# Kernel optimization log

Measured on AMD Instinct MI355X. Metric: run time of the kernel, lower is better.

## Reference

```python
import jax, jax.numpy as jnp
import numpy as np

E = 30      # embedding_dim
H = 3       # num_heads
D = E // H  # head_dim = 10
EPS = 1e-5


def setup_inputs() -> dict:
    key = jax.random.key(0)
    ks = jax.random.split(key, 16)
    B = 1_000_000
    s = 0.1
    return {
        "input": jax.random.normal(ks[0], (B, 2, 5), dtype=jnp.float32),
        "w_emb": jax.random.normal(ks[1], (E, 5), dtype=jnp.float32) * s,
        "b_emb": jax.random.normal(ks[2], (E,), dtype=jnp.float32) * s,
        "w_in": jax.random.normal(ks[3], (3 * E, E), dtype=jnp.float32) * s,
        "b_in": jax.random.normal(ks[4], (3 * E,), dtype=jnp.float32) * s,
        "w_out": jax.random.normal(ks[5], (E, E), dtype=jnp.float32) * s,
        "b_out": jax.random.normal(ks[6], (E,), dtype=jnp.float32) * s,
        "w1": jax.random.normal(ks[7], (E, E), dtype=jnp.float32) * s,
        "b1": jax.random.normal(ks[8], (E,), dtype=jnp.float32) * s,
        "w2": jax.random.normal(ks[9], (E, E), dtype=jnp.float32) * s,
        "b2": jax.random.normal(ks[10], (E,), dtype=jnp.float32) * s,
        "gamma": jnp.ones((E,), dtype=jnp.float32),
        "beta": jnp.zeros((E,), dtype=jnp.float32),
        "w_o": jax.random.normal(ks[11], (3, E), dtype=jnp.float32) * s,
        "b_o": jax.random.normal(ks[12], (3,), dtype=jnp.float32) * s,
    }


def _layernorm(x, gamma, beta):
    mu = jnp.mean(x, axis=-1, keepdims=True)
    var = jnp.var(x, axis=-1, keepdims=True)
    return (x - mu) * jax.lax.rsqrt(var + EPS) * gamma + beta


def reference(input, w_emb, b_emb, w_in, b_in, w_out, b_out,
              w1, b1, w2, b2, gamma, beta, w_o, b_o):
    B = input.shape[0]
    # embed both tokens: [B,2,5] -> [B,2,E], exact (erf) GELU as in torch default
    x = jax.nn.gelu(jnp.einsum('bse,de->bsd', input, w_emb) + b_emb,
                    approximate=False)
    # MHA (torch nn.MultiheadAttention, batch_first)
    qkv = jnp.einsum('bsd,fd->bsf', x, w_in) + b_in  # [B,2,3E]
    q, k, v = jnp.split(qkv, 3, axis=-1)
    # [B,2,E] -> [B,H,2,D]
    q = q.reshape(B, 2, H, D).transpose(0, 2, 1, 3)
    k = k.reshape(B, 2, H, D).transpose(0, 2, 1, 3)
    v = v.reshape(B, 2, H, D).transpose(0, 2, 1, 3)
    scores = jnp.einsum('bhqd,bhkd->bhqk', q, k) / jnp.sqrt(jnp.float32(D))
    attn = jax.nn.softmax(scores, axis=-1)
    ctx = jnp.einsum('bhqk,bhkd->bhqd', attn, v)  # [B,H,2,D]
    ctx = ctx.transpose(0, 2, 1, 3).reshape(B, 2, E)
    attn_out = jnp.einsum('bsd,fd->bsf', ctx, w_out) + b_out
    out = _layernorm(attn_out + x, gamma, beta)
    # FFN (applied per token, same weights)
    h = jax.nn.gelu(jnp.einsum('bsd,fd->bsf', out, w1) + b1, approximate=False)
    fc_out = jnp.einsum('bsd,fd->bsf', h, w2) + b2
    out = _layernorm(out + fc_out, gamma, beta)  # same norm1 params reused
    logits = jnp.einsum('bsd,od->bso', out, w_o) + b_o
    return logits[:, 1, :]
```

## Files before the change

kernel.cpp:

```cpp
#include <hip/hip_runtime.h>
#include <math.h>


typedef _Float16 h8 __attribute__((ext_vector_type(8)));
typedef _Float16 h2v __attribute__((ext_vector_type(2)));
typedef float f4 __attribute__((ext_vector_type(4)));
typedef f4 f4u __attribute__((aligned(4)));

#define EPS 1e-5f
#define GDEG 9

struct GeluCU { unsigned c[GDEG + 2]; };

__device__ __forceinline__ f4 MF(h8 a, h8 b, f4 c) {
    return __builtin_amdgcn_mfma_f32_16x16x32_f16(a, b, c, 0, 0, 0);
}

struct GeluC { h2v c[GDEG + 1]; h2v k2; };

__device__ __forceinline__ h2v gelu2(float lo, float hi, const GeluC& gc,
                                     h2v P3, h2v N3) {
    h2v x = __builtin_bit_cast(h2v, __builtin_amdgcn_cvt_pkrtz(lo, hi));
    h2v xc = __builtin_elementwise_min(__builtin_elementwise_max(x, N3), P3);
    h2v t = xc * xc;
    h2v s = t * gc.k2 - (_Float16)1.0f;
    h2v p = gc.c[GDEG];
    #pragma unroll
    for (int i = GDEG - 1; i >= 0; --i) p = p * s + gc.c[i];
    h2v w = xc * p;
    return x * w + x * (_Float16)0.5f;
}

__device__ __forceinline__ h8 pack_b(f4 t0, f4 t1, bool g3) {
    union { unsigned u[4]; h8 v; } r;
    r.u[0] = __builtin_bit_cast(unsigned, __builtin_amdgcn_cvt_pkrtz(t0[0], t0[1]));
    r.u[1] = __builtin_bit_cast(unsigned, __builtin_amdgcn_cvt_pkrtz(t0[2], t0[3]));
    r.u[2] = __builtin_bit_cast(unsigned, __builtin_amdgcn_cvt_pkrtz(t1[0], t1[1]));
    r.u[3] = g3 ? 0x3C00u
                : __builtin_bit_cast(unsigned, __builtin_amdgcn_cvt_pkrtz(t1[2], t1[3]));
    return r.v;
}

__global__ void prep(const float* __restrict__ w_emb, const float* __restrict__ b_emb,
                     const float* __restrict__ w_in,  const float* __restrict__ b_in,
                     const float* __restrict__ w_out, const float* __restrict__ b_out,
                     const float* __restrict__ w1,    const float* __restrict__ b1,
                     const float* __restrict__ w2,    const float* __restrict__ b2,
                     const float* __restrict__ gamma, const float* __restrict__ beta,
                     const float* __restrict__ w_o,   const float* __restrict__ b_o,
                     unsigned short* __restrict__ ws) {
    int t = blockIdx.x * 256 + threadIdx.x;
    const float S = 0.31622776601683794f;
    if (t < 960) {
        int tile = t >> 6, lane = t & 63;
        int g = lane >> 4;
        int mat = (tile == 14) ? 7 : (tile >> 1);
        int row = (tile & 1) * 16 + (lane & 15);
        #pragma unroll
        for (int e = 0; e < 8; ++e) {
            int k = (e < 4) ? (4 * g + e) : (16 + 4 * g + (e - 4));
            float v = 0.f;
            switch (mat) {
              case 0: if (row<30) { if (k<5)  v = w_emb[row*5+k];        else if (k==30) v = b_emb[row]; } break;
              case 1: if (row<30) { if (k<30) v = w_in[row*30+k]*S;      else if (k==30) v = b_in[row]*S; } break;
              case 2: if (row<30) { if (k<30) v = w_in[(30+row)*30+k];   else if (k==30) v = b_in[30+row]; } break;
              case 3: if (row<30) { if (k<30) v = w_in[(60+row)*30+k];   else if (k==30) v = b_in[60+row]; } break;
              case 4: if (row<30) { if (k<30) v = w_out[row*30+k];       else if (k==30) v = b_out[row]; } break;
              case 5: if (row<30) { if (k<30) v = w1[row*30+k];          else if (k==30) v = b1[row]; } break;
              case 6: if (row<30) { if (k<30) v = w2[row*30+k];          else if (k==30) v = b2[row]; } break;
              case 7: if (row<3)  { if (k<30) v = w_o[row*30+k];         else if (k==30) v = b_o[row]; } break;
            }
            _Float16 hv = (_Float16)v;
            ws[tile * 512 + lane * 8 + e] = __builtin_bit_cast(unsigned short, hv);
        }
    } else if (t < 1024) {
        int f = t - 960;
        float* tab = (float*)(ws + 15 * 512);
        if (f < 32) tab[f] = (f < 30) ? gamma[f] : 0.f;
        else        tab[f] = (f - 32 < 30) ? beta[f - 32] : 0.f;
    }
}

#define RED2(x) { x += __shfl_xor(x, 16); x += __shfl_xor(x, 32); }

#define ITERS 8

__global__ __launch_bounds__(256, 3) void model_kernel(
    const float* __restrict__ input,
    const unsigned short* __restrict__ ws,
    float* __restrict__ out, int B, GeluCU gcu)
{
    const int lane = threadIdx.x & 63;
    const int wv   = threadIdx.x >> 6;
    const int c    = lane & 15;
    const int g    = lane >> 4;
    const bool g3  = (g == 3);
    const f4 Z = {0.f, 0.f, 0.f, 0.f};

    const h8* wsf = (const h8*)ws;
    h8 Aemb0 = wsf[0*64+lane],  Aemb1 = wsf[1*64+lane];
    h8 Aq0   = wsf[2*64+lane],  Aq1   = wsf[3*64+lane];
    h8 Ak0   = wsf[4*64+lane],  Ak1   = wsf[5*64+lane];
    h8 Av0   = wsf[6*64+lane],  Av1   = wsf[7*64+lane];
    h8 Ao0   = wsf[8*64+lane],  Ao1   = wsf[9*64+lane];
    h8 A10   = wsf[10*64+lane], A11   = wsf[11*64+lane];
    h8 A20   = wsf[12*64+lane], A21   = wsf[13*64+lane];
    h8 Awo   = wsf[14*64+lane];

    const float* tab = (const float*)(ws + 15 * 512);
    f4 gaV0 = *(const f4*)&tab[4*g];
    f4 gaV1 = *(const f4*)&tab[16+4*g];
    f4 beV0 = *(const f4*)&tab[32+4*g];
    f4 beV1 = *(const f4*)&tab[48+4*g];

    GeluC gc;
    #pragma unroll
    for (int i = 0; i <= GDEG; ++i) gc.c[i] = __builtin_bit_cast(h2v, gcu.c[i]);
    gc.k2 = __builtin_bit_cast(h2v, gcu.c[GDEG + 1]);
    const h2v P3 = {(_Float16)3.0f, (_Float16)3.0f};
    const h2v N3 = {(_Float16)-3.0f, (_Float16)-3.0f};

    f4 m0v, m1v;
    #pragma unroll
    for (int r = 0; r < 4; ++r) {
        m0v[r] = (4 * g + r) < 10 ? 1.f : 0.f;
        m1v[r] = (16 + 4 * g + r) < 20 ? 1.f : 0.f;
    }

    const int base_it = (blockIdx.x * 4 + wv) * ITERS;
    {
        int e0 = base_it * 16 + c; if (e0 > B - 1) e0 = B - 1;
    }
    const float* ip0;
    {
        int e0 = base_it * 16 + c; if (e0 > B - 1) e0 = B - 1;
        ip0 = input + (long)e0 * 10;
    }
    f4u va = *(const f4u*)ip0;        float v4 = ip0[4];
    f4u vb = *(const f4u*)(ip0 + 5);  float v9 = ip0[9];

    for (int it = 0; it < ITERS; ++it) {
        const int eb = (base_it + it) * 16;

        union { unsigned u[4]; h8 v; } bi0, bi1;
        unsigned pk01a = __builtin_bit_cast(unsigned, __builtin_amdgcn_cvt_pkrtz(va[0], va[1]));
        unsigned pk23a = __builtin_bit_cast(unsigned, __builtin_amdgcn_cvt_pkrtz(va[2], va[3]));
        unsigned pk4a  = __builtin_bit_cast(unsigned, __builtin_amdgcn_cvt_pkrtz(v4, 0.f));
        unsigned pk01b = __builtin_bit_cast(unsigned, __builtin_amdgcn_cvt_pkrtz(vb[0], vb[1]));
        unsigned pk23b = __builtin_bit_cast(unsigned, __builtin_amdgcn_cvt_pkrtz(vb[2], vb[3]));
        unsigned pk4b  = __builtin_bit_cast(unsigned, __builtin_amdgcn_cvt_pkrtz(v9, 0.f));
        bi0.u[0] = (g == 0) ? pk01a : ((g == 1) ? pk4a : 0u);
        bi0.u[1] = (g == 0) ? pk23a : 0u;
        bi0.u[2] = 0u;
        bi0.u[3] = g3 ? 0x3C00u : 0u;
        bi1.u[0] = (g == 0) ? pk01b : ((g == 1) ? pk4b : 0u);
        bi1.u[1] = (g == 0) ? pk23b : 0u;
        bi1.u[2] = 0u;
        bi1.u[3] = g3 ? 0x3C00u : 0u;

        {
            int itn = (it + 1 < ITERS) ? (it + 1) : it;
            int en = (base_it + itn) * 16 + c; if (en > B - 1) en = B - 1;
            const float* ipn = input + (long)en * 10;
            va = *(const f4u*)ipn;        v4 = ipn[4];
            vb = *(const f4u*)(ipn + 5);  v9 = ipn[9];
        }

        f4 x0t0p = MF(Aemb0, bi0.v, Z);
        f4 x0t1p = MF(Aemb1, bi0.v, Z);
        f4 x1t0p = MF(Aemb0, bi1.v, Z);
        f4 x1t1p = MF(Aemb1, bi1.v, Z);

        h2v gx00 = gelu2(x0t0p[0], x0t0p[1], gc, P3, N3);
        h2v gx01 = gelu2(x0t0p[2], x0t0p[3], gc, P3, N3);
        h2v gx02 = gelu2(x0t1p[0], x0t1p[1], gc, P3, N3);
        h2v gx03 = gelu2(x0t1p[2], x0t1p[3], gc, P3, N3);
        h2v gx10 = gelu2(x1t0p[0], x1t0p[1], gc, P3, N3);
        h2v gx11 = gelu2(x1t0p[2], x1t0p[3], gc, P3, N3);
        h2v gx12 = gelu2(x1t1p[0], x1t1p[1], gc, P3, N3);
        h2v gx13 = gelu2(x1t1p[2], x1t1p[3], gc, P3, N3);

        union { unsigned u[4]; h8 v; } Bx0, Bx1;
        Bx0.u[0] = __builtin_bit_cast(unsigned, gx00);
        Bx0.u[1] = __builtin_bit_cast(unsigned, gx01);
        Bx0.u[2] = __builtin_bit_cast(unsigned, gx02);
        Bx0.u[3] = g3 ? 0x3C00u : __builtin_bit_cast(unsigned, gx03);
        Bx1.u[0] = __builtin_bit_cast(unsigned, gx10);
        Bx1.u[1] = __builtin_bit_cast(unsigned, gx11);
        Bx1.u[2] = __builtin_bit_cast(unsigned, gx12);
        Bx1.u[3] = g3 ? 0x3C00u : __builtin_bit_cast(unsigned, gx13);

        f4 x1t0, x1t1;
        x1t0[0]=(float)gx10[0]; x1t0[1]=(float)gx10[1]; x1t0[2]=(float)gx11[0]; x1t0[3]=(float)gx11[1];
        x1t1[0]=(float)gx12[0]; x1t1[1]=(float)gx12[1]; x1t1[2]=(float)gx13[0]; x1t1[3]=(float)gx13[1];

        f4 q0t  = MF(Aq0, Bx1.v, Z), q1t  = MF(Aq1, Bx1.v, Z);
        f4 k0t0 = MF(Ak0, Bx0.v, Z), k0t1 = MF(Ak1, Bx0.v, Z);
        f4 k1t0 = MF(Ak0, Bx1.v, Z), k1t1 = MF(Ak1, Bx1.v, Z);
        f4 v0t0 = MF(Av0, Bx0.v, Z), v0t1 = MF(Av1, Bx0.v, Z);
        f4 v1t0 = MF(Av0, Bx1.v, Z), v1t1 = MF(Av1, Bx1.v, Z);

        float tA0=0.f, tA1=0.f, tB0=0.f, tB1=0.f;
        float s0h0=0.f, s1h0=0.f, b0h1=0.f, b1h1=0.f;
        #pragma unroll
        for (int r = 0; r < 4; ++r) {
            float p00 = q0t[r]*k0t0[r], p10 = q0t[r]*k1t0[r];
            float p01 = q1t[r]*k0t1[r], p11 = q1t[r]*k1t1[r];
            tA0 += p00; s0h0 = fmaf(p00, m0v[r], s0h0);
            tA1 += p10; s1h0 = fmaf(p10, m0v[r], s1h0);
            tB0 += p01; b0h1 = fmaf(p01, m1v[r], b0h1);
            tB1 += p11; b1h1 = fmaf(p11, m1v[r], b1h1);
        }
        float s0h1 = tA0 - s0h0 + b0h1;
        float s0h2 = tB0 - b0h1;
        float s1h1 = tA1 - s1h0 + b1h1;
        float s1h2 = tB1 - b1h1;
        RED2(s0h0); RED2(s0h1); RED2(s0h2);
        RED2(s1h0); RED2(s1h1); RED2(s1h2);

        float e00 = __expf(s0h0), e10 = __expf(s1h0);
        float e01 = __expf(s0h1), e11 = __expf(s1h1);
        float e02 = __expf(s0h2), e12 = __expf(s1h2);
        float i0 = 1.f/(e00+e10), i1 = 1.f/(e01+e11), i2 = 1.f/(e02+e12);
        float a0h0 = e00*i0, a1h0 = e10*i0;
        float a0h1 = e01*i1, a1h1 = e11*i1;
        float a0h2 = e02*i2, a1h2 = e12*i2;
        float dA0 = a0h0-a0h1, dA1 = a1h0-a1h1;
        float dB0 = a0h1-a0h2, dB1 = a1h1-a1h2;

        f4 ctx0, ctx1;
        #pragma unroll
        for (int r = 0; r < 4; ++r) {
            float A0 = fmaf(m0v[r], dA0, a0h1), A1 = fmaf(m0v[r], dA1, a1h1);
            ctx0[r] = fmaf(A1, v1t0[r], A0 * v0t0[r]);
            float B0 = fmaf(m1v[r], dB0, a0h2), B1 = fmaf(m1v[r], dB1, a1h2);
            ctx1[r] = fmaf(B1, v1t1[r], B0 * v0t1[r]);
        }

        h8 Bc = pack_b(ctx0, ctx1, g3);
        f4 t0 = MF(Ao0, Bc, x1t0);
        f4 t1 = MF(Ao1, Bc, x1t1);

        float s = 0.f, ss = 0.f;
        #pragma unroll
        for (int r = 0; r < 4; ++r) {
            s  += t0[r] + t1[r];
            ss += t0[r]*t0[r] + t1[r]*t1[r];
        }
        RED2(s); RED2(ss);
        float mu = s * (1.f/30.f);
        float rs = rsqrtf(ss * (1.f/30.f) - mu*mu + EPS);
        f4 y0, y1;
        #pragma unroll
        for (int r = 0; r < 4; ++r) {
            y0[r] = fmaf((t0[r]-mu)*rs, gaV0[r], beV0[r]);
            y1[r] = fmaf((t1[r]-mu)*rs, gaV1[r], beV1[r]);
        }

        h8 By = pack_b(y0, y1, g3);
        f4 hh0p = MF(A10, By, Z), hh1p = MF(A11, By, Z);
        h2v gh0 = gelu2(hh0p[0], hh0p[1], gc, P3, N3);
        h2v gh1 = gelu2(hh0p[2], hh0p[3], gc, P3, N3);
        h2v gh2 = gelu2(hh1p[0], hh1p[1], gc, P3, N3);
        h2v gh3 = gelu2(hh1p[2], hh1p[3], gc, P3, N3);
        union { unsigned u[4]; h8 v; } Bh;
        Bh.u[0] = __builtin_bit_cast(unsigned, gh0);
        Bh.u[1] = __builtin_bit_cast(unsigned, gh1);
        Bh.u[2] = __builtin_bit_cast(unsigned, gh2);
        Bh.u[3] = g3 ? 0x3C00u : __builtin_bit_cast(unsigned, gh3);

        f4 u0 = MF(A20, Bh.v, y0), u1 = MF(A21, Bh.v, y1);

        s = 0.f; ss = 0.f;
        #pragma unroll
        for (int r = 0; r < 4; ++r) {
            s  += u0[r] + u1[r];
            ss += u0[r]*u0[r] + u1[r]*u1[r];
        }
        RED2(s); RED2(ss);
        mu = s * (1.f/30.f);
        rs = rsqrtf(ss * (1.f/30.f) - mu*mu + EPS);
        f4 w0, w1;
        #pragma unroll
        for (int r = 0; r < 4; ++r) {
            w0[r] = fmaf((u0[r]-mu)*rs, gaV0[r], beV0[r]);
            w1[r] = fmaf((u1[r]-mu)*rs, gaV1[r], beV1[r]);
        }

        h8 Bw = pack_b(w0, w1, g3);
        f4 lg = MF(Awo, Bw, Z);
        if (g == 0 && eb + c < B) {
            long base = (long)(eb + c) * 3;
            out[base]     = lg[0];
            out[base + 1] = lg[1];
            out[base + 2] = lg[2];
        }
    }
}

static unsigned short f32_to_f16(float f) {
    unsigned x;
    __builtin_memcpy(&x, &f, 4);
    unsigned sign = (x >> 16) & 0x8000u;
    int exp = (int)((x >> 23) & 0xFFu) - 127 + 15;
    unsigned mant = x & 0x7FFFFFu;
    if (exp <= 0) {
        if (exp < -10) return (unsigned short)sign;
        mant |= 0x800000u;
        unsigned shift = (unsigned)(1 - exp) + 13;
        unsigned half = mant >> shift;
        unsigned rem = mant & ((1u << shift) - 1);
        unsigned halfway = 1u << (shift - 1);
        if (rem > halfway || (rem == halfway && (half & 1))) half++;
        return (unsigned short)(sign | half);
    }
    if (exp >= 31) return (unsigned short)(sign | 0x7C00u);
    unsigned half = sign | ((unsigned)exp << 10) | (mant >> 13);
    unsigned rem = mant & 0x1FFFu;
    if (rem > 0x1000u || (rem == 0x1000u && (half & 1))) half++;
    return (unsigned short)half;
}

extern "C" void kernel_launch(void* const* d_in, const int* in_sizes, int n_in,
                              void* d_out, int out_size, void* d_ws, size_t ws_size,
                              hipStream_t stream) {
    const float* input = (const float*)d_in[0];
    const float* w_emb = (const float*)d_in[1];
    const float* b_emb = (const float*)d_in[2];
    const float* w_in  = (const float*)d_in[3];
    const float* b_in  = (const float*)d_in[4];
    const float* w_out = (const float*)d_in[5];
    const float* b_out = (const float*)d_in[6];
    const float* w1    = (const float*)d_in[7];
    const float* b1    = (const float*)d_in[8];
    const float* w2    = (const float*)d_in[9];
    const float* b2    = (const float*)d_in[10];
    const float* gamma = (const float*)d_in[11];
    const float* beta  = (const float*)d_in[12];
    const float* w_o   = (const float*)d_in[13];
    const float* b_o   = (const float*)d_in[14];
    float* out = (float*)d_out;
    unsigned short* ws = (unsigned short*)d_ws;

    const int B = in_sizes[0] / 10;

    GeluCU gcu;
    {
        const int NN = 64;
        double a[GDEG + 1];
        for (int j = 0; j <= GDEG; ++j) a[j] = 0.0;
        for (int k = 0; k < NN; ++k) {
            double th = M_PI * (k + 0.5) / NN;
            double sx = cos(th);
            double u  = 4.5 * (sx + 1.0);
            double z  = sqrt(u);
            double Phi = 0.5 * (1.0 + erf(z * 0.7071067811865476));
            double Gv  = (z > 1e-8) ? (Phi - 0.5) / z : 0.3989422804014327;
            for (int j = 0; j <= GDEG; ++j) a[j] += Gv * cos(j * th);
        }
        for (int j = 0; j <= GDEG; ++j) a[j] *= 2.0 / NN;
        a[0] *= 0.5;
        double Tm[GDEG + 1][GDEG + 1];
        for (int i = 0; i <= GDEG; ++i)
            for (int j = 0; j <= GDEG; ++j) Tm[i][j] = 0.0;
        Tm[0][0] = 1.0; Tm[1][1] = 1.0;
        for (int k2 = 2; k2 <= GDEG; ++k2)
            for (int i = 0; i <= GDEG; ++i) {
                double v = -Tm[k2 - 2][i];
                if (i > 0) v += 2.0 * Tm[k2 - 1][i - 1];
                Tm[k2][i] = v;
            }
        for (int i = 0; i <= GDEG; ++i) {
            double m = 0.0;
            for (int j = 0; j <= GDEG; ++j) m += a[j] * Tm[j][i];
            unsigned short us = f32_to_f16((float)m);
            gcu.c[i] = (unsigned)us * 0x10001u;
        }
        unsigned short ku = f32_to_f16(2.0f / 9.0f);
        gcu.c[GDEG + 1] = (unsigned)ku * 0x10001u;
    }

    prep<<<4, 256, 0, stream>>>(w_emb, b_emb, w_in, b_in, w_out, b_out,
                                w1, b1, w2, b2, gamma, beta, w_o, b_o, ws);

    const int per_block = 4 * ITERS * 16;
    const int blocks = (B + per_block - 1) / per_block;
    model_kernel<<<blocks, 256, 0, stream>>>(input, ws, out, B, gcu);
}
```

Measured before the change: 74.80 us.

## Stage weight tiles in LDS and reload per iteration to raise occupancy

Copies the fp16 weight tiles and the gamma/beta table into shared memory once per block. Most A-operand fragments and the layernorm vectors are then reloaded from LDS right before each use, with an asm barrier so the compiler cannot hoist them back into registers. Only the Q/K/V weights stay register-resident. This cuts VGPR pressure so launch bounds can rise from 3 to 4 waves per SIMD, at the cost of extra LDS traffic each iteration and a block-wide copy plus sync at startup.

```diff
diff --git a/kernel.cpp b/kernel.cpp
--- a/kernel.cpp
+++ b/kernel.cpp
@@ -85,11 +85,24 @@
 
 #define ITERS 8
 
-__global__ __launch_bounds__(256, 3) void model_kernel(
+__device__ __forceinline__ h8 ldw(const unsigned short* lws, int tile, int lane) {
+    unsigned off = (unsigned)(tile * 512 + lane * 8);
+    asm volatile("" : "+v"(off));
+    return *(const h8*)(lws + off);
+}
+__device__ __forceinline__ f4 ldt(const float* tabl, int idx) {
+    unsigned off = (unsigned)idx;
+    asm volatile("" : "+v"(off));
+    return *(const f4*)(tabl + off);
+}
+
+__global__ __launch_bounds__(256, 4) void model_kernel(
     const float* __restrict__ input,
     const unsigned short* __restrict__ ws,
     float* __restrict__ out, int B, GeluCU gcu)
 {
+    __shared__ unsigned short lws[15 * 512 + 128];
+
     const int lane = threadIdx.x & 63;
     const int wv   = threadIdx.x >> 6;
     const int c    = lane & 15;
@@ -97,21 +110,15 @@
     const bool g3  = (g == 3);
     const f4 Z = {0.f, 0.f, 0.f, 0.f};
 
+    for (int i = threadIdx.x; i < 15 * 512 + 128; i += 256) lws[i] = ws[i];
+    __syncthreads();
+
     const h8* wsf = (const h8*)ws;
-    h8 Aemb0 = wsf[0*64+lane],  Aemb1 = wsf[1*64+lane];
-    h8 Aq0   = wsf[2*64+lane],  Aq1   = wsf[3*64+lane];
-    h8 Ak0   = wsf[4*64+lane],  Ak1   = wsf[5*64+lane];
-    h8 Av0   = wsf[6*64+lane],  Av1   = wsf[7*64+lane];
-    h8 Ao0   = wsf[8*64+lane],  Ao1   = wsf[9*64+lane];
-    h8 A10   = wsf[10*64+lane], A11   = wsf[11*64+lane];
-    h8 A20   = wsf[12*64+lane], A21   = wsf[13*64+lane];
-    h8 Awo   = wsf[14*64+lane];
-
-    const float* tab = (const float*)(ws + 15 * 512);
-    f4 gaV0 = *(const f4*)&tab[4*g];
-    f4 gaV1 = *(const f4*)&tab[16+4*g];
-    f4 beV0 = *(const f4*)&tab[32+4*g];
-    f4 beV1 = *(const f4*)&tab[48+4*g];
+    h8 Aq0 = wsf[2*64+lane], Aq1 = wsf[3*64+lane];
+    h8 Ak0 = wsf[4*64+lane], Ak1 = wsf[5*64+lane];
+    h8 Av0 = wsf[6*64+lane], Av1 = wsf[7*64+lane];
+
+    const float* tabl = (const float*)(lws + 15 * 512);
 
     GeluC gc;
     #pragma unroll
@@ -128,9 +135,6 @@
     }
 
     const int base_it = (blockIdx.x * 4 + wv) * ITERS;
-    {
-        int e0 = base_it * 16 + c; if (e0 > B - 1) e0 = B - 1;
-    }
     const float* ip0;
     {
         int e0 = base_it * 16 + c; if (e0 > B - 1) e0 = B - 1;
@@ -166,6 +170,8 @@
             vb = *(const f4u*)(ipn + 5);  v9 = ipn[9];
         }
 
+        h8 Aemb0 = ldw(lws, 0, lane);
+        h8 Aemb1 = ldw(lws, 1, lane);
         f4 x0t0p = MF(Aemb0, bi0.v, Z);
         f4 x0t1p = MF(Aemb1, bi0.v, Z);
         f4 x1t0p = MF(Aemb0, bi1.v, Z);
@@ -238,6 +244,8 @@
         }
 
         h8 Bc = pack_b(ctx0, ctx1, g3);
+        h8 Ao0 = ldw(lws, 8, lane);
+        h8 Ao1 = ldw(lws, 9, lane);
         f4 t0 = MF(Ao0, Bc, x1t0);
         f4 t1 = MF(Ao1, Bc, x1t1);
 
@@ -248,6 +256,10 @@
             ss += t0[r]*t0[r] + t1[r]*t1[r];
         }
         RED2(s); RED2(ss);
+        f4 gaV0 = ldt(tabl, 4*g);
+        f4 gaV1 = ldt(tabl, 16+4*g);
+        f4 beV0 = ldt(tabl, 32+4*g);
+        f4 beV1 = ldt(tabl, 48+4*g);
         float mu = s * (1.f/30.f);
         float rs = rsqrtf(ss * (1.f/30.f) - mu*mu + EPS);
         f4 y0, y1;
@@ -258,6 +270,8 @@
         }
 
         h8 By = pack_b(y0, y1, g3);
+        h8 A10 = ldw(lws, 10, lane);
+        h8 A11 = ldw(lws, 11, lane);
         f4 hh0p = MF(A10, By, Z), hh1p = MF(A11, By, Z);
         h2v gh0 = gelu2(hh0p[0], hh0p[1], gc, P3, N3);
         h2v gh1 = gelu2(hh0p[2], hh0p[3], gc, P3, N3);
@@ -269,6 +283,8 @@
         Bh.u[2] = __builtin_bit_cast(unsigned, gh2);
         Bh.u[3] = g3 ? 0x3C00u : __builtin_bit_cast(unsigned, gh3);
 
+        h8 A20 = ldw(lws, 12, lane);
+        h8 A21 = ldw(lws, 13, lane);
         f4 u0 = MF(A20, Bh.v, y0), u1 = MF(A21, Bh.v, y1);
 
         s = 0.f; ss = 0.f;
@@ -288,6 +304,7 @@
         }
 
         h8 Bw = pack_b(w0, w1, g3);
+        h8 Awo = ldw(lws, 14, lane);
         f4 lg = MF(Awo, Bw, Z);
         if (g == 0 && eb + c < B) {
             long base = (long)(eb + c) * 3;
```

Measured after the change: 79.14 us. 1.06x slower.
